# Kernel optimization log

Measured on AMD Instinct MI355X. Metric: run time of the kernel, lower is better.

Reference implementation:

```python
import jax, jax.numpy as jnp
import numpy as np

B, S, D = 2, 4096, 512   # batch, seq_len, input_dim
W, H = 256, 4            # memory width (d_model), attention heads
DH = W // H              # per-head depth


def _dense(x, w, b):
    return x @ w + b


def setup_inputs() -> dict:
    key = jax.random.key(0)
    ks = jax.random.split(key, 24)
    def w(k, shape):
        return jax.random.normal(k, shape, dtype=jnp.float32) * 0.02
    inp = {
        "x": jax.random.normal(ks[0], (B, S, D), dtype=jnp.float32),
        # outer q/k/v projections D -> W
        "qp_w": w(ks[1], (D, W)), "qp_b": jnp.zeros((W,), jnp.float32),
        "kp_w": w(ks[2], (D, W)), "kp_b": jnp.zeros((W,), jnp.float32),
        "vp_w": w(ks[3], (D, W)), "vp_b": jnp.zeros((W,), jnp.float32),
        # MHA internal projections W -> W
        "wq_w": w(ks[4], (W, W)), "wq_b": jnp.zeros((W,), jnp.float32),
        "wk_w": w(ks[5], (W, W)), "wk_b": jnp.zeros((W,), jnp.float32),
        "wv_w": w(ks[6], (W, W)), "wv_b": jnp.zeros((W,), jnp.float32),
        "wo_w": w(ks[7], (W, W)), "wo_b": jnp.zeros((W,), jnp.float32),
        # deep MLP memory (depth=2, gelu) + its output proj W -> W
        "m0_w": w(ks[8], (W, W)), "m0_b": jnp.zeros((W,), jnp.float32),
        "m1_w": w(ks[9], (W, W)), "m1_b": jnp.zeros((W,), jnp.float32),
        "mo_w": w(ks[10], (W, W)), "mo_b": jnp.zeros((W,), jnp.float32),
        # final output projection W -> D
        "op_w": w(ks[11], (W, D)), "op_b": jnp.zeros((D,), jnp.float32),
    }
    return inp


def reference(x, qp_w, qp_b, kp_w, kp_b, vp_w, vp_b,
              wq_w, wq_b, wk_w, wk_b, wv_w, wv_b, wo_w, wo_b,
              m0_w, m0_b, m1_w, m1_b, mo_w, mo_b, op_w, op_b):
    # outer projections (D -> W)
    q0 = _dense(x, qp_w, qp_b)
    k0 = _dense(x, kp_w, kp_b)
    v0 = _dense(x, vp_w, vp_b)
    # MHA internal projections (W -> W)
    q = _dense(q0, wq_w, wq_b)
    k = _dense(k0, wk_w, wk_b)
    v = _dense(v0, wv_w, wv_b)
    # split heads: [B,S,W] -> [B,H,S,DH]
    def split(t):
        return t.reshape(B, S, H, DH).transpose(0, 2, 1, 3)
    qh, kh, vh = split(q), split(k), split(v)
    scores = jnp.einsum('bhqd,bhkd->bhqk', qh, kh) / jnp.sqrt(jnp.float32(DH))
    attn = jax.nn.softmax(scores, axis=-1)
    ctx = jnp.einsum('bhqk,bhkd->bhqd', attn, vh)
    ctx = ctx.transpose(0, 2, 1, 3).reshape(B, S, W)
    retrieved = _dense(ctx, wo_w, wo_b)
    # deep MLP memory (exact gelu, matching keras 'gelu')
    h = jax.nn.gelu(_dense(retrieved, m0_w, m0_b), approximate=False)
    h = jax.nn.gelu(_dense(h, m1_w, m1_b), approximate=False)
    mem = _dense(h, mo_w, mo_b)
    # final projection + residual
    out = _dense(mem, op_w, op_b) + x
    return out
```

## Files before the change

kernel.cpp:

```cpp
#include <hip/hip_runtime.h>
#include <cstdint>
#include <cstddef>


#define GAS(p) ((const __attribute__((address_space(1))) void*)(p))
#define LAS(p) ((__attribute__((address_space(3))) void*)(p))

typedef __attribute__((ext_vector_type(8))) short bfrag;
typedef __attribute__((ext_vector_type(4))) float facc;
typedef __attribute__((ext_vector_type(16))) float facc16;
typedef uint16_t u16;

__device__ __forceinline__ u16 f2bf(float f) {
  uint32_t u = __float_as_uint(f);
  u += 0x7fffu + ((u >> 16) & 1u);
  return (u16)(u >> 16);
}
__device__ __forceinline__ float bf2f(u16 h) {
  return __uint_as_float((uint32_t)h << 16);
}
__device__ __forceinline__ float fast_exp2(float x) {
  float r;
  asm("v_exp_f32 %0, %1" : "=v"(r) : "v"(x));
  return r;
}
__device__ __forceinline__ float fast_rcp(float x) {
  float r;
  asm("v_rcp_f32 %0, %1" : "=v"(r) : "v"(x));
  return r;
}
__device__ __forceinline__ float gelu_fast(float v) {
  float y = v * 0.7978845608028654f * (1.f + 0.044715f * v * v);
  float e = fast_exp2(y * 2.8853900817779268f);
  float t = (e - 1.f) * fast_rcp(e + 1.f);
  return 0.5f * v * (1.f + t);
}
__device__ __forceinline__ facc mfma16(bfrag a, bfrag b, facc c) {
  return __builtin_amdgcn_mfma_f32_16x16x32_bf16(a, b, c, 0, 0, 0);
}
__device__ __forceinline__ facc16 mfma32(bfrag a, bfrag b, facc16 c) {
  return __builtin_amdgcn_mfma_f32_32x32x16_bf16(a, b, c, 0, 0, 0);
}

union U4 { uint32_t w[4]; bfrag f; };

__device__ __forceinline__ bfrag lds_frag(const u16* lds, int row, int kk, int ln) {
  int kb  = (kk << 6) + ((ln >> 4) << 4);
  int off = (row << 7) + (kb ^ ((row & 7) << 4));
  return *(const bfrag*)((const char*)lds + off);
}

template <int ROWS, int NW>
__device__ __forceinline__ void stage_tile(const u16* gbase, int ldK, u16* lds,
                                           int wv, int ln) {
#pragma unroll
  for (int i = 0; i < ROWS / 8 / NW; i++) {
    int seg = i * NW + wv;
    int row = (seg << 3) + (ln >> 3);
    int kb  = (ln & 7) << 4;
    const char* g = (const char*)(gbase + (size_t)row * ldK) +
                    (kb ^ ((row & 7) << 4));
    __builtin_amdgcn_global_load_lds(GAS(g), LAS(lds + (seg << 9)), 16, 0, 0);
  }
}

template <int EPI, int BN>
__global__ __launch_bounds__(256) void gemm_bt(
    const u16* __restrict__ A, const u16* __restrict__ Bt,
    const float* __restrict__ bias, const float* __restrict__ resid,
    u16* __restrict__ obf, float* __restrict__ of32,
    u16* __restrict__ qb, u16* __restrict__ kb2, u16* __restrict__ vb,
    int M, int N, int K) {
  const int t = threadIdx.x, wv = t >> 6, ln = t & 63;
  const int wr = wv >> 1, wc = wv & 1;
  const int m0 = blockIdx.y << 7, n0 = blockIdx.x * BN;
  constexpr int NJ = (BN + 31) / 32;

  __shared__ __align__(16) u16 Al[128 * 64];
  __shared__ __align__(16) u16 Bl[BN * 64];

  facc acc[4][NJ];
#pragma unroll
  for (int i = 0; i < 4; i++)
#pragma unroll
    for (int j = 0; j < NJ; j++)
#pragma unroll
      for (int r = 0; r < 4; r++) acc[i][j][r] = 0.f;

  const u16* Ab = A + (size_t)m0 * K;
  const u16* Bb = Bt + (size_t)n0 * K;
  stage_tile<128, 4>(Ab, K, Al, wv, ln);
  stage_tile<BN, 4>(Bb, K, Bl, wv, ln);

  const int nk = K >> 6;
  for (int kt = 0; kt < nk; ++kt) {
    __syncthreads();
#pragma unroll
    for (int kk = 0; kk < 2; kk++) {
      bfrag av[4], bv[NJ];
#pragma unroll
      for (int i = 0; i < 4; i++)
        av[i] = lds_frag(Al, (wr << 6) + (i << 4) + (ln & 15), kk, ln);
#pragma unroll
      for (int j = 0; j < NJ; j++)
        bv[j] = lds_frag(Bl, wc * (BN / 2) + (j << 4) + (ln & 15), kk, ln);
      __builtin_amdgcn_s_setprio(1);
#pragma unroll
      for (int i = 0; i < 4; i++)
#pragma unroll
        for (int j = 0; j < NJ; j++)
          acc[i][j] = mfma16(av[i], bv[j], acc[i][j]);
      __builtin_amdgcn_s_setprio(0);
    }
    if (kt + 1 < nk) {
      __syncthreads();
      stage_tile<128, 4>(Ab + (kt + 1) * 64, K, Al, wv, ln);
      stage_tile<BN, 4>(Bb + (kt + 1) * 64, K, Bl, wv, ln);
    }
  }

  const int rb = (ln >> 4) << 2, cb = ln & 15;
#pragma unroll
  for (int i = 0; i < 4; i++) {
#pragma unroll
    for (int j = 0; j < NJ; j++) {
      const int col = n0 + wc * (BN / 2) + (j << 4) + cb;
      const float bcol = bias ? bias[col] : 0.f;
#pragma unroll
      for (int r = 0; r < 4; r++) {
        const int row = m0 + (wr << 6) + (i << 4) + rb + r;
        float val = acc[i][j][r] + bcol;
        if (EPI == 0) {
          obf[(size_t)row * N + col] = f2bf(val);
        } else if (EPI == 1) {
          obf[(size_t)row * N + col] = f2bf(gelu_fast(val));
        } else if (EPI == 2) {
          const int sec = col >> 8, cc = col & 255, h = cc >> 6, dh = cc & 63;
          const int b = row >> 12, s = row & 4095;
          const int bh = b * 4 + h;
          if (sec == 0) {
            qb[((size_t)bh * 4096 + s) * 64 + dh] =
                f2bf(val * 0.18033688011112042f);
          } else if (sec == 1) {
            const int kt2 = s >> 5, kl = s & 31;
            const int dc = dh >> 4, lane = kl + ((dh >> 3) & 1) * 32, e = dh & 7;
            kb2[((size_t)bh * 128 + kt2) * 2048 + dc * 512 + lane * 8 + e] =
                f2bf(val);
          } else {
            const int kt2 = s >> 5, c = (s >> 4) & 1;
            const int lane = ((s >> 3) & 1) * 32 + (dh & 31), e = s & 7;
            const int dj = dh >> 5;
            vb[((size_t)bh * 128 + kt2) * 2048 + (c * 2 + dj) * 512 +
               lane * 8 + e] = f2bf(val);
          }
        } else {
          of32[(size_t)row * N + col] = val + resid[(size_t)row * N + col];
        }
      }
    }
  }
}

__global__ __launch_bounds__(256) void wgemm5(
    const u16* __restrict__ wqkvT, const u16* __restrict__ owqkv,
    const u16* __restrict__ m0_t, const u16* __restrict__ wo_bf,
    const u16* __restrict__ opT, const u16* __restrict__ mo_bf,
    u16* __restrict__ Wqkv_t, u16* __restrict__ Wf1_t,
    u16* __restrict__ Wmo_t) {
  const int z = blockIdx.z;
  const u16 *A, *Bt; u16* out; int M, N, rowOff;
  if (z < 3)      { A = wqkvT + z * 65536; Bt = owqkv + z * 131072;
                    out = Wqkv_t; M = 256; N = 512; rowOff = z * 256; }
  else if (z == 3){ A = m0_t; Bt = wo_bf; out = Wf1_t; M = 256; N = 256; rowOff = 0; }
  else            { A = opT;  Bt = mo_bf; out = Wmo_t; M = 512; N = 256; rowOff = 0; }
  const int m0 = blockIdx.y << 7, n0 = blockIdx.x << 6;
  if (m0 >= M || n0 >= N) return;

  const int t = threadIdx.x, wv = t >> 6, ln = t & 63;
  const int wr = wv >> 1, wc = wv & 1;
  __shared__ __align__(16) u16 Al[128 * 64];
  __shared__ __align__(16) u16 Bl[64 * 64];

  facc acc[4][2];
#pragma unroll
  for (int i = 0; i < 4; i++)
#pragma unroll
    for (int j = 0; j < 2; j++)
#pragma unroll
      for (int r = 0; r < 4; r++) acc[i][j][r] = 0.f;

  const u16* Ab = A + (size_t)m0 * 256;
  const u16* Bb = Bt + (size_t)n0 * 256;
  stage_tile<128, 4>(Ab, 256, Al, wv, ln);
  stage_tile<64, 4>(Bb, 256, Bl, wv, ln);

  for (int kt = 0; kt < 4; ++kt) {
    __syncthreads();
#pragma unroll
    for (int kk = 0; kk < 2; kk++) {
      bfrag av[4], bv[2];
#pragma unroll
      for (int i = 0; i < 4; i++)
        av[i] = lds_frag(Al, (wr << 6) + (i << 4) + (ln & 15), kk, ln);
#pragma unroll
      for (int j = 0; j < 2; j++)
        bv[j] = lds_frag(Bl, wc * 32 + (j << 4) + (ln & 15), kk, ln);
#pragma unroll
      for (int i = 0; i < 4; i++)
#pragma unroll
        for (int j = 0; j < 2; j++)
          acc[i][j] = mfma16(av[i], bv[j], acc[i][j]);
    }
    if (kt + 1 < 4) {
      __syncthreads();
      stage_tile<128, 4>(Ab + (kt + 1) * 64, 256, Al, wv, ln);
      stage_tile<64, 4>(Bb + (kt + 1) * 64, 256, Bl, wv, ln);
    }
  }

  const int rb = (ln >> 4) << 2, cb = ln & 15;
#pragma unroll
  for (int i = 0; i < 4; i++)
#pragma unroll
    for (int j = 0; j < 2; j++) {
      const int col = n0 + wc * 32 + (j << 4) + cb;
#pragma unroll
      for (int r = 0; r < 4; r++) {
        const int row = m0 + (wr << 6) + (i << 4) + rb + r;
        out[(size_t)(rowOff + row) * N + col] = f2bf(acc[i][j][r]);
      }
    }
}

__global__ __launch_bounds__(128) void attn5(
    const u16* __restrict__ qg, const u16* __restrict__ kfg,
    const u16* __restrict__ vfg, u16* __restrict__ Opart,
    float* __restrict__ lpart, int NT) {
  const int t = threadIdx.x, wv = t >> 6, ln = t & 63;
  const int l31 = ln & 31, lh = ln >> 5;
  const int qt = blockIdx.x, bh = blockIdx.y, kv = blockIdx.z;
  const int qbase = qt * 128 + wv * 64;
  const u16* Q  = qg + ((size_t)bh * 4096 + qbase) * 64;
  const u16* Kf = kfg + ((size_t)bh * 128 + (size_t)kv * NT) * 2048;
  const u16* Vf = vfg + ((size_t)bh * 128 + (size_t)kv * NT) * 2048;

  __shared__ __align__(16) u16 Klds[2][2048];
  __shared__ __align__(16) u16 Vlds[2][2048];

  bfrag qf[2][4];
#pragma unroll
  for (int qi = 0; qi < 2; qi++) {
    const u16* qp = Q + (size_t)(((qi << 5) + l31) << 6) + (lh << 3);
#pragma unroll
    for (int dc = 0; dc < 4; dc++)
      qf[qi][dc] = *(const bfrag*)(qp + (dc << 4));
  }

  facc16 oacc[2][2];
#pragma unroll
  for (int qi = 0; qi < 2; qi++)
#pragma unroll
    for (int r = 0; r < 16; r++) { oacc[qi][0][r] = 0.f; oacc[qi][1][r] = 0.f; }
  float lsum0 = 0.f, lsum1 = 0.f;

  {
    const u16* src = wv ? Vf : Kf;
    u16* dst = wv ? Vlds[0] : Klds[0];
#pragma unroll
    for (int i = 0; i < 4; i++)
      __builtin_amdgcn_global_load_lds(GAS(src + i * 512 + ln * 8),
                                       LAS(dst + i * 512), 16, 0, 0);
  }

  for (int kt = 0; kt < NT; ++kt) {
    const int cur = kt & 1;
    __syncthreads();
    if (kt + 1 < NT) {
      const u16* src = (wv ? Vf : Kf) + (size_t)(kt + 1) * 2048;
      u16* dst = wv ? Vlds[cur ^ 1] : Klds[cur ^ 1];
#pragma unroll
      for (int i = 0; i < 4; i++)
        __builtin_amdgcn_global_load_lds(GAS(src + i * 512 + ln * 8),
                                         LAS(dst + i * 512), 16, 0, 0);
    }
    bfrag kf[4];
#pragma unroll
    for (int dc = 0; dc < 4; dc++)
      kf[dc] = *(const bfrag*)(Klds[cur] + dc * 512 + ln * 8);

    bfrag pa[2][2];
#pragma unroll
    for (int qi = 0; qi < 2; qi++) {
      facc16 sa;
#pragma unroll
      for (int r = 0; r < 16; r++) sa[r] = 0.f;
      __builtin_amdgcn_s_setprio(1);
#pragma unroll
      for (int dc = 0; dc < 4; dc++)
        sa = mfma32(kf[dc], qf[qi][dc], sa);
      __builtin_amdgcn_s_setprio(0);
      float p[16];
      float ls = 0.f;
#pragma unroll
      for (int r = 0; r < 16; r++) { p[r] = fast_exp2(sa[r]); ls += p[r]; }
      if (qi == 0) lsum0 += ls; else lsum1 += ls;
      uint32_t u0, u1, u2, u3, u4, u5, u6, u7;
      asm("v_cvt_pk_bf16_f32 %0, %1, %2" : "=v"(u0) : "v"(p[0]),  "v"(p[1]));
      asm("v_cvt_pk_bf16_f32 %0, %1, %2" : "=v"(u1) : "v"(p[2]),  "v"(p[3]));
      asm("v_cvt_pk_bf16_f32 %0, %1, %2" : "=v"(u2) : "v"(p[4]),  "v"(p[5]));
      asm("v_cvt_pk_bf16_f32 %0, %1, %2" : "=v"(u3) : "v"(p[6]),  "v"(p[7]));
      asm("v_cvt_pk_bf16_f32 %0, %1, %2" : "=v"(u4) : "v"(p[8]),  "v"(p[9]));
      asm("v_cvt_pk_bf16_f32 %0, %1, %2" : "=v"(u5) : "v"(p[10]), "v"(p[11]));
      asm("v_cvt_pk_bf16_f32 %0, %1, %2" : "=v"(u6) : "v"(p[12]), "v"(p[13]));
      asm("v_cvt_pk_bf16_f32 %0, %1, %2" : "=v"(u7) : "v"(p[14]), "v"(p[15]));
      asm volatile("v_permlane32_swap_b32 %0, %1" : "+v"(u0), "+v"(u2));
      asm volatile("v_permlane32_swap_b32 %0, %1" : "+v"(u1), "+v"(u3));
      asm volatile("v_permlane32_swap_b32 %0, %1" : "+v"(u4), "+v"(u6));
      asm volatile("v_permlane32_swap_b32 %0, %1" : "+v"(u5), "+v"(u7));
      U4 c0; c0.w[0] = u0; c0.w[1] = u1; c0.w[2] = u2; c0.w[3] = u3;
      U4 c1; c1.w[0] = u4; c1.w[1] = u5; c1.w[2] = u6; c1.w[3] = u7;
      pa[qi][0] = c0.f;
      pa[qi][1] = c1.f;
    }
#pragma unroll
    for (int c = 0; c < 2; c++) {
      bfrag vf0 = *(const bfrag*)(Vlds[cur] + (c * 2 + 0) * 512 + ln * 8);
      bfrag vf1 = *(const bfrag*)(Vlds[cur] + (c * 2 + 1) * 512 + ln * 8);
      __builtin_amdgcn_s_setprio(1);
      oacc[0][0] = mfma32(pa[0][c], vf0, oacc[0][0]);
      oacc[1][0] = mfma32(pa[1][c], vf0, oacc[1][0]);
      oacc[0][1] = mfma32(pa[0][c], vf1, oacc[0][1]);
      oacc[1][1] = mfma32(pa[1][c], vf1, oacc[1][1]);
      __builtin_amdgcn_s_setprio(0);
    }
  }

  lsum0 += __shfl_xor(lsum0, 32);
  lsum1 += __shfl_xor(lsum1, 32);

  const size_t obase = ((size_t)kv * 8 + bh) * 4096 + qbase;
#pragma unroll
  for (int qi = 0; qi < 2; qi++) {
#pragma unroll
    for (int r = 0; r < 16; r++) {
      const int qrow = (qi << 5) + (r & 3) + ((r >> 2) << 3) + (lh << 2);
#pragma unroll
      for (int dj = 0; dj < 2; dj++)
        Opart[(obase + qrow) * 64 + (dj << 5) + l31] = f2bf(oacc[qi][dj][r]);
    }
    if (lh == 0)
      lpart[obase + (qi << 5) + l31] = qi == 0 ? lsum0 : lsum1;
  }
}

__global__ __launch_bounds__(256) void attn_combineN(
    const u16* __restrict__ Opart, const float* __restrict__ lpart,
    u16* __restrict__ ctx, int np) {
  const int idx = blockIdx.x * 256 + threadIdx.x;
  const int d0 = (idx & 7) << 3, s = (idx >> 3) & 4095, bh = idx >> 15;
  const size_t sb = (size_t)bh * 4096 + s;
  float acc[8] = {0.f, 0.f, 0.f, 0.f, 0.f, 0.f, 0.f, 0.f};
  float lsum = 0.f;
  for (int pz = 0; pz < np; pz++) {
    const size_t pb = (size_t)pz * 8 * 4096;
    bfrag a = *(const bfrag*)(Opart + (pb + sb) * 64 + d0);
#pragma unroll
    for (int j = 0; j < 8; j++) acc[j] += bf2f((u16)a[j]);
    lsum += lpart[pb + sb];
  }
  const float rl = 1.f / lsum;
  bfrag o;
#pragma unroll
  for (int j = 0; j < 8; j++) o[j] = (short)f2bf(acc[j] * rl);
  *(bfrag*)(ctx + ((size_t)(bh >> 2) * 4096 + s) * 256 + ((bh & 3) << 6) + d0) = o;
}

__global__ __launch_bounds__(256) void prep_all(
    const float* __restrict__ x,
    const float* __restrict__ qp, const float* __restrict__ kp,
    const float* __restrict__ vp, const float* __restrict__ mo,
    const float* __restrict__ wo,
    const float* __restrict__ wq, const float* __restrict__ wk,
    const float* __restrict__ wv, const float* __restrict__ m0,
    const float* __restrict__ m1, const float* __restrict__ op_w,
    const float* __restrict__ qp_b, const float* __restrict__ kp_b,
    const float* __restrict__ vp_b, const float* __restrict__ wq_b,
    const float* __restrict__ wk_b, const float* __restrict__ wv_b,
    const float* __restrict__ mo_b, const float* __restrict__ op_b,
    const float* __restrict__ wo_b, const float* __restrict__ m0_b,
    u16* __restrict__ xb, u16* __restrict__ owqkv, u16* __restrict__ mo_bf,
    u16* __restrict__ wo_bf, u16* __restrict__ wqkvT, u16* __restrict__ m0_t,
    u16* __restrict__ m1_t, u16* __restrict__ opT,
    float* __restrict__ bqkv, float* __restrict__ bmo,
    float* __restrict__ bf1) {
  const int bid = blockIdx.x, t = threadIdx.x;
  if (bid < 2048) {
    const size_t i = ((size_t)bid * 256 + t) * 8;
    float4 a = *(const float4*)(x + i);
    float4 b = *(const float4*)(x + i + 4);
    bfrag o;
    o[0] = (short)f2bf(a.x); o[1] = (short)f2bf(a.y);
    o[2] = (short)f2bf(a.z); o[3] = (short)f2bf(a.w);
    o[4] = (short)f2bf(b.x); o[5] = (short)f2bf(b.y);
    o[6] = (short)f2bf(b.z); o[7] = (short)f2bf(b.w);
    *(bfrag*)(xb + i) = o;
  } else if (bid < 2176) {
    const int i = (bid - 2048) * 4096 + t * 16;
    const float* s; u16* dst; int off;
    if (i < 131072)      { s = qp; dst = owqkv;          off = i; }
    else if (i < 262144) { s = kp; dst = owqkv + 131072; off = i - 131072; }
    else if (i < 393216) { s = vp; dst = owqkv + 262144; off = i - 262144; }
    else if (i < 458752) { s = mo; dst = mo_bf;          off = i - 393216; }
    else                 { s = wo; dst = wo_bf;          off = i - 458752; }
    bfrag o0, o1;
#pragma unroll
    for (int q = 0; q < 2; q++) {
      float4 v0 = *(const float4*)(s + off + q * 8);
      float4 v1 = *(const float4*)(s + off + q * 8 + 4);
      bfrag& o = q ? o1 : o0;
      o[0] = (short)f2bf(v0.x); o[1] = (short)f2bf(v0.y);
      o[2] = (short)f2bf(v0.z); o[3] = (short)f2bf(v0.w);
      o[4] = (short)f2bf(v1.x); o[5] = (short)f2bf(v1.y);
      o[6] = (short)f2bf(v1.z); o[7] = (short)f2bf(v1.w);
    }
    *(bfrag*)(dst + off) = o0;
    *(bfrag*)(dst + off + 8) = o1;
  } else if (bid < 2288) {
    __shared__ float tile[64][65];
    const int tid = bid - 2176;
    const float* src; u16* dst; int r0, c0, ldS, ldD;
    if (tid < 80) {
      const int mi = tid >> 4, tt = tid & 15;
      r0 = ((tt >> 2) << 6); c0 = ((tt & 3) << 6); ldS = 256; ldD = 256;
      switch (mi) {
        case 0: src = wq; dst = wqkvT; break;
        case 1: src = wk; dst = wqkvT + 65536; break;
        case 2: src = wv; dst = wqkvT + 131072; break;
        case 3: src = m0; dst = m0_t; break;
        default: src = m1; dst = m1_t; break;
      }
    } else {
      const int tt = tid - 80;
      r0 = ((tt >> 3) << 6); c0 = ((tt & 7) << 6);
      ldS = 512; ldD = 256; src = op_w; dst = opT;
    }
    {
      const int r = t >> 2, cc = (t & 3) << 4;
      const float* sp = src + (size_t)(r0 + r) * ldS + c0 + cc;
#pragma unroll
      for (int q = 0; q < 4; q++) {
        float4 v = *(const float4*)(sp + q * 4);
        tile[r][cc + q * 4 + 0] = v.x; tile[r][cc + q * 4 + 1] = v.y;
        tile[r][cc + q * 4 + 2] = v.z; tile[r][cc + q * 4 + 3] = v.w;
      }
    }
    __syncthreads();
    {
      const int cl = t >> 2, k16 = (t & 3) << 4;
      bfrag o0, o1;
#pragma unroll
      for (int j = 0; j < 8; j++) {
        o0[j] = (short)f2bf(tile[k16 + j][cl]);
        o1[j] = (short)f2bf(tile[k16 + 8 + j][cl]);
      }
      u16* dp = dst + (size_t)(c0 + cl) * ldD + r0 + k16;
      *(bfrag*)(dp) = o0;
      *(bfrag*)(dp + 8) = o1;
    }
  } else {
    const int bz = bid - 2288;
    if (bz < 3) {
      const float* ob = bz == 0 ? qp_b : (bz == 1 ? kp_b : vp_b);
      const float* iw = bz == 0 ? wq : (bz == 1 ? wk : wv);
      const float* ib = bz == 0 ? wq_b : (bz == 1 ? wk_b : wv_b);
      float s = 0.f;
      for (int c = 0; c < 256; c++) s += ob[c] * iw[(size_t)c * 256 + t];
      bqkv[bz * 256 + t] = s + ib[t];
    } else if (bz < 5) {
      const int d = (bz - 3) * 256 + t;
      float s = 0.f;
      for (int c = 0; c < 256; c++) s += mo_b[c] * op_w[(size_t)c * 512 + d];
      bmo[d] = s + op_b[d];
    } else {
      float s = 0.f;
      for (int c = 0; c < 256; c++) s += wo_b[c] * m0[(size_t)c * 256 + t];
      bf1[t] = s + m0_b[t];
    }
  }
}

extern "C" void kernel_launch(void* const* d_in, const int* in_sizes, int n_in,
                              void* d_out, int out_size, void* d_ws,
                              size_t ws_size, hipStream_t stream) {
  const float* x    = (const float*)d_in[0];
  const float* qp_w = (const float*)d_in[1];
  const float* qp_b = (const float*)d_in[2];
  const float* kp_w = (const float*)d_in[3];
  const float* kp_b = (const float*)d_in[4];
  const float* vp_w = (const float*)d_in[5];
  const float* vp_b = (const float*)d_in[6];
  const float* wq_w = (const float*)d_in[7];
  const float* wq_b = (const float*)d_in[8];
  const float* wk_w = (const float*)d_in[9];
  const float* wk_b = (const float*)d_in[10];
  const float* wv_w = (const float*)d_in[11];
  const float* wv_b = (const float*)d_in[12];
  const float* wo_w = (const float*)d_in[13];
  const float* wo_b = (const float*)d_in[14];
  const float* m0_w = (const float*)d_in[15];
  const float* m0_b = (const float*)d_in[16];
  const float* m1_w = (const float*)d_in[17];
  const float* m1_b = (const float*)d_in[18];
  const float* mo_w = (const float*)d_in[19];
  const float* mo_b = (const float*)d_in[20];
  const float* op_w = (const float*)d_in[21];
  const float* op_b = (const float*)d_in[22];
  float* out = (float*)d_out;

  const size_t MB = 1024 * 1024;
  const int kvs = (ws_size >= 56 * MB) ? 8 : 4;
  const int NT = 128 / kvs;

  char* ws = (char*)d_ws;
  u16*   q_buf  = (u16*)(ws);
  u16*   kf_buf = (u16*)(ws + 4 * MB);
  u16*   vf_buf = (u16*)(ws + 8 * MB);
  u16*   ctx    = (u16*)(ws + 12 * MB);
  u16*   xb     = (u16*)(ws + 16 * MB);
  u16*   Opart  = (u16*)(ws + 16 * MB);
  char*  wb     = ws + 16 * MB + (size_t)kvs * 4 * MB;
  u16*   owqkv  = (u16*)(wb);
  u16*   wqkvT  = (u16*)(wb + 786432);
  u16*   Wqkv_t = (u16*)(wb + 1179648);
  u16*   m0_t   = (u16*)(wb + 1966080);
  u16*   m1_t   = (u16*)(wb + 2097152);
  u16*   opT    = (u16*)(wb + 2228224);
  u16*   mo_bf  = (u16*)(wb + 2490368);
  u16*   wo_bf  = (u16*)(wb + 2621440);
  u16*   Wf1_t  = (u16*)(wb + 2752512);
  u16*   Wmo_t  = (u16*)(wb + 2883584);
  float* bqkv   = (float*)(wb + 3145728);
  float* bmo    = (float*)(wb + 3149824);
  float* bf1    = (float*)(wb + 3151872);
  float* lpart  = (float*)(wb + 3153920);
  u16* h1 = q_buf;
  u16* h2 = kf_buf;

  prep_all<<<2294, 256, 0, stream>>>(
      x, qp_w, kp_w, vp_w, mo_w, wo_w,
      wq_w, wk_w, wv_w, m0_w, m1_w, op_w,
      qp_b, kp_b, vp_b, wq_b, wk_b, wv_b, mo_b, op_b, wo_b, m0_b,
      xb, owqkv, mo_bf, wo_bf, wqkvT, m0_t, m1_t, opT, bqkv, bmo, bf1);
  wgemm5<<<dim3(8, 4, 5), 256, 0, stream>>>(
      wqkvT, owqkv, m0_t, wo_bf, opT, mo_bf, Wqkv_t, Wf1_t, Wmo_t);

  gemm_bt<2, 64><<<dim3(12, 64), 256, 0, stream>>>(
      xb, Wqkv_t, bqkv, nullptr, nullptr, nullptr, q_buf, kf_buf, vf_buf,
      8192, 768, 512);
  attn5<<<dim3(32, 8, kvs), 128, 0, stream>>>(q_buf, kf_buf, vf_buf,
                                              Opart, lpart, NT);
  attn_combineN<<<1024, 256, 0, stream>>>(Opart, lpart, ctx, kvs);

  gemm_bt<1, 32><<<dim3(8, 64), 256, 0, stream>>>(
      ctx, Wf1_t, bf1, nullptr, h1, nullptr, nullptr, nullptr, nullptr,
      8192, 256, 256);
  gemm_bt<1, 32><<<dim3(8, 64), 256, 0, stream>>>(
      h1, m1_t, m1_b, nullptr, h2, nullptr, nullptr, nullptr, nullptr,
      8192, 256, 256);
  gemm_bt<3, 64><<<dim3(8, 64), 256, 0, stream>>>(
      h2, Wmo_t, bmo, x, nullptr, out, nullptr, nullptr, nullptr,
      8192, 512, 256);
}
```

Before: 223.1 us.

## Use single-wave attention blocks with vmcnt waits and MFMA row sums

Each attention block is reduced from two waves to one. That single wave now loads both its K and V tiles into LDS itself, and __syncthreads is replaced by explicit s_waitcnt vmcnt counting for the double buffer. The softmax row sums are no longer accumulated with VALU adds and a cross-lane shuffle; they come from extra MFMAs of P against a ones fragment, which also changes how lpart is written. This removes block barriers and VALU work but doubles the grid, and each block now issues more loads per wave and duplicates the K/V LDS traffic.

```diff
diff --git a/kernel.cpp b/kernel.cpp
--- a/kernel.cpp
+++ b/kernel.cpp
@@ -232,14 +232,14 @@
     }
 }
 
-__global__ __launch_bounds__(128) void attn5(
+__global__ __launch_bounds__(64) void attn7(
     const u16* __restrict__ qg, const u16* __restrict__ kfg,
     const u16* __restrict__ vfg, u16* __restrict__ Opart,
     float* __restrict__ lpart, int NT) {
-  const int t = threadIdx.x, wv = t >> 6, ln = t & 63;
+  const int ln = threadIdx.x;
   const int l31 = ln & 31, lh = ln >> 5;
   const int qt = blockIdx.x, bh = blockIdx.y, kv = blockIdx.z;
-  const int qbase = qt * 128 + wv * 64;
+  const int qbase = qt * 64;
   const u16* Q  = qg + ((size_t)bh * 4096 + qbase) * 64;
   const u16* Kf = kfg + ((size_t)bh * 128 + (size_t)kv * NT) * 2048;
   const u16* Vf = vfg + ((size_t)bh * 128 + (size_t)kv * NT) * 2048;
@@ -255,34 +255,47 @@
     for (int dc = 0; dc < 4; dc++)
       qf[qi][dc] = *(const bfrag*)(qp + (dc << 4));
   }
+  bfrag ones;
+#pragma unroll
+  for (int j = 0; j < 8; j++) ones[j] = (short)0x3F80;
 
   facc16 oacc[2][2];
+  facc16 lacc[2];
 #pragma unroll
   for (int qi = 0; qi < 2; qi++)
 #pragma unroll
-    for (int r = 0; r < 16; r++) { oacc[qi][0][r] = 0.f; oacc[qi][1][r] = 0.f; }
-  float lsum0 = 0.f, lsum1 = 0.f;
-
-  {
-    const u16* src = wv ? Vf : Kf;
-    u16* dst = wv ? Vlds[0] : Klds[0];
-#pragma unroll
-    for (int i = 0; i < 4; i++)
-      __builtin_amdgcn_global_load_lds(GAS(src + i * 512 + ln * 8),
-                                       LAS(dst + i * 512), 16, 0, 0);
-  }
+    for (int r = 0; r < 16; r++) {
+      oacc[qi][0][r] = 0.f; oacc[qi][1][r] = 0.f; lacc[qi][r] = 0.f;
+    }
+
+#pragma unroll
+  for (int i = 0; i < 4; i++)
+    __builtin_amdgcn_global_load_lds(GAS(Kf + i * 512 + ln * 8),
+                                     LAS(Klds[0] + i * 512), 16, 0, 0);
+#pragma unroll
+  for (int i = 0; i < 4; i++)
+    __builtin_amdgcn_global_load_lds(GAS(Vf + i * 512 + ln * 8),
+                                     LAS(Vlds[0] + i * 512), 16, 0, 0);
 
   for (int kt = 0; kt < NT; ++kt) {
     const int cur = kt & 1;
-    __syncthreads();
     if (kt + 1 < NT) {
-      const u16* src = (wv ? Vf : Kf) + (size_t)(kt + 1) * 2048;
-      u16* dst = wv ? Vlds[cur ^ 1] : Klds[cur ^ 1];
+      const u16* ksrc = Kf + (size_t)(kt + 1) * 2048;
+      const u16* vsrc = Vf + (size_t)(kt + 1) * 2048;
 #pragma unroll
       for (int i = 0; i < 4; i++)
-        __builtin_amdgcn_global_load_lds(GAS(src + i * 512 + ln * 8),
-                                         LAS(dst + i * 512), 16, 0, 0);
-    }
+        __builtin_amdgcn_global_load_lds(GAS(ksrc + i * 512 + ln * 8),
+                                         LAS(Klds[cur ^ 1] + i * 512), 16, 0, 0);
+#pragma unroll
+      for (int i = 0; i < 4; i++)
+        __builtin_amdgcn_global_load_lds(GAS(vsrc + i * 512 + ln * 8),
+                                         LAS(Vlds[cur ^ 1] + i * 512), 16, 0, 0);
+      asm volatile("s_waitcnt vmcnt(8)" ::: "memory");
+    } else {
+      asm volatile("s_waitcnt vmcnt(0)" ::: "memory");
+    }
+    __builtin_amdgcn_sched_barrier(0);
+
     bfrag kf[4];
 #pragma unroll
     for (int dc = 0; dc < 4; dc++)
@@ -300,10 +313,8 @@
         sa = mfma32(kf[dc], qf[qi][dc], sa);
       __builtin_amdgcn_s_setprio(0);
       float p[16];
-      float ls = 0.f;
-#pragma unroll
-      for (int r = 0; r < 16; r++) { p[r] = fast_exp2(sa[r]); ls += p[r]; }
-      if (qi == 0) lsum0 += ls; else lsum1 += ls;
+#pragma unroll
+      for (int r = 0; r < 16; r++) p[r] = fast_exp2(sa[r]);
       uint32_t u0, u1, u2, u3, u4, u5, u6, u7;
       asm("v_cvt_pk_bf16_f32 %0, %1, %2" : "=v"(u0) : "v"(p[0]),  "v"(p[1]));
       asm("v_cvt_pk_bf16_f32 %0, %1, %2" : "=v"(u1) : "v"(p[2]),  "v"(p[3]));
@@ -331,12 +342,11 @@
       oacc[1][0] = mfma32(pa[1][c], vf0, oacc[1][0]);
       oacc[0][1] = mfma32(pa[0][c], vf1, oacc[0][1]);
       oacc[1][1] = mfma32(pa[1][c], vf1, oacc[1][1]);
+      lacc[0] = mfma32(pa[0][c], ones, lacc[0]);
+      lacc[1] = mfma32(pa[1][c], ones, lacc[1]);
       __builtin_amdgcn_s_setprio(0);
     }
   }
-
-  lsum0 += __shfl_xor(lsum0, 32);
-  lsum1 += __shfl_xor(lsum1, 32);
 
   const size_t obase = ((size_t)kv * 8 + bh) * 4096 + qbase;
 #pragma unroll
@@ -347,9 +357,8 @@
 #pragma unroll
       for (int dj = 0; dj < 2; dj++)
         Opart[(obase + qrow) * 64 + (dj << 5) + l31] = f2bf(oacc[qi][dj][r]);
-    }
-    if (lh == 0)
-      lpart[obase + (qi << 5) + l31] = qi == 0 ? lsum0 : lsum1;
+      if (l31 == 0) lpart[obase + qrow] = lacc[qi][r];
+    }
   }
 }
 
@@ -557,8 +566,8 @@
   gemm_bt<2, 64><<<dim3(12, 64), 256, 0, stream>>>(
       xb, Wqkv_t, bqkv, nullptr, nullptr, nullptr, q_buf, kf_buf, vf_buf,
       8192, 768, 512);
-  attn5<<<dim3(32, 8, kvs), 128, 0, stream>>>(q_buf, kf_buf, vf_buf,
-                                              Opart, lpart, NT);
+  attn7<<<dim3(64, 8, kvs), 64, 0, stream>>>(q_buf, kf_buf, vf_buf,
+                                             Opart, lpart, NT);
   attn_combineN<<<1024, 256, 0, stream>>>(Opart, lpart, ctx, kvs);
 
   gemm_bt<1, 32><<<dim3(8, 64), 256, 0, stream>>>(
```

Result: slower. 229.5 us (+2.9%).

## Replace LDS-staged attention with single-wave kernel loading K/V fragments directly to registers

Applied to the files above, without the earlier changes.

The attention kernel drops its shared-memory double buffer and block barriers. Each single-wavefront block now loads K and V fragments straight from global memory into registers, with a two-deep register ping-pong that prefetches the next tile while the current one is computed. The grid doubles in the query dimension so each block still covers 64 queries. This removes the LDS round trip and __syncthreads, but K/V are no longer shared between two waves, so global/L2 traffic for K/V doubles and register pressure rises. The loop also assumes NT is even, since the second step in each iteration runs unconditionally.

```diff
diff --git a/kernel.cpp b/kernel.cpp
--- a/kernel.cpp
+++ b/kernel.cpp
@@ -232,21 +232,75 @@
     }
 }
 
-__global__ __launch_bounds__(128) void attn5(
+#define LOAD_KV(kf_, vf_, kt_)                                               \
+  do {                                                                       \
+    const u16* kp_ = Kf + (size_t)(kt_) * 2048 + (ln << 3);                  \
+    const u16* vp_ = Vf + (size_t)(kt_) * 2048 + (ln << 3);                  \
+    _Pragma("unroll")                                                        \
+    for (int i_ = 0; i_ < 4; i_++) kf_[i_] = *(const bfrag*)(kp_ + i_ * 512);\
+    _Pragma("unroll")                                                        \
+    for (int i_ = 0; i_ < 4; i_++) vf_[i_] = *(const bfrag*)(vp_ + i_ * 512);\
+  } while (0)
+
+#define ATTN_TILE_STEP(kf_, vf_)                                             \
+  do {                                                                       \
+    bfrag pa[2][2];                                                          \
+    _Pragma("unroll")                                                        \
+    for (int qi = 0; qi < 2; qi++) {                                         \
+      facc16 sa;                                                             \
+      _Pragma("unroll")                                                      \
+      for (int r = 0; r < 16; r++) sa[r] = 0.f;                              \
+      __builtin_amdgcn_s_setprio(1);                                         \
+      _Pragma("unroll")                                                      \
+      for (int dc = 0; dc < 4; dc++)                                         \
+        sa = mfma32(kf_[dc], qf[qi][dc], sa);                                \
+      __builtin_amdgcn_s_setprio(0);                                         \
+      float p[16];                                                           \
+      float ls = 0.f;                                                        \
+      _Pragma("unroll")                                                      \
+      for (int r = 0; r < 16; r++) { p[r] = fast_exp2(sa[r]); ls += p[r]; }  \
+      if (qi == 0) lsum0 += ls; else lsum1 += ls;                            \
+      uint32_t u0, u1, u2, u3, u4, u5, u6, u7;                               \
+      asm("v_cvt_pk_bf16_f32 %0, %1, %2" : "=v"(u0) : "v"(p[0]),  "v"(p[1]));\
+      asm("v_cvt_pk_bf16_f32 %0, %1, %2" : "=v"(u1) : "v"(p[2]),  "v"(p[3]));\
+      asm("v_cvt_pk_bf16_f32 %0, %1, %2" : "=v"(u2) : "v"(p[4]),  "v"(p[5]));\
+      asm("v_cvt_pk_bf16_f32 %0, %1, %2" : "=v"(u3) : "v"(p[6]),  "v"(p[7]));\
+      asm("v_cvt_pk_bf16_f32 %0, %1, %2" : "=v"(u4) : "v"(p[8]),  "v"(p[9]));\
+      asm("v_cvt_pk_bf16_f32 %0, %1, %2" : "=v"(u5) : "v"(p[10]), "v"(p[11]));\
+      asm("v_cvt_pk_bf16_f32 %0, %1, %2" : "=v"(u6) : "v"(p[12]), "v"(p[13]));\
+      asm("v_cvt_pk_bf16_f32 %0, %1, %2" : "=v"(u7) : "v"(p[14]), "v"(p[15]));\
+      asm volatile("v_permlane32_swap_b32 %0, %1" : "+v"(u0), "+v"(u2));     \
+      asm volatile("v_permlane32_swap_b32 %0, %1" : "+v"(u1), "+v"(u3));     \
+      asm volatile("v_permlane32_swap_b32 %0, %1" : "+v"(u4), "+v"(u6));     \
+      asm volatile("v_permlane32_swap_b32 %0, %1" : "+v"(u5), "+v"(u7));     \
+      U4 c0; c0.w[0] = u0; c0.w[1] = u1; c0.w[2] = u2; c0.w[3] = u3;         \
+      U4 c1; c1.w[0] = u4; c1.w[1] = u5; c1.w[2] = u6; c1.w[3] = u7;         \
+      pa[qi][0] = c0.f;                                                      \
+      pa[qi][1] = c1.f;                                                      \
+    }                                                                        \
+    _Pragma("unroll")                                                        \
+    for (int c = 0; c < 2; c++) {                                            \
+      __builtin_amdgcn_s_setprio(1);                                         \
+      oacc[0][0] = mfma32(pa[0][c], vf_[c * 2 + 0], oacc[0][0]);             \
+      oacc[1][0] = mfma32(pa[1][c], vf_[c * 2 + 0], oacc[1][0]);             \
+      oacc[0][1] = mfma32(pa[0][c], vf_[c * 2 + 1], oacc[0][1]);             \
+      oacc[1][1] = mfma32(pa[1][c], vf_[c * 2 + 1], oacc[1][1]);             \
+      __builtin_amdgcn_s_setprio(0);                                         \
+    }                                                                        \
+  } while (0)
+
+__global__ __launch_bounds__(64) void attn8(
     const u16* __restrict__ qg, const u16* __restrict__ kfg,
     const u16* __restrict__ vfg, u16* __restrict__ Opart,
     float* __restrict__ lpart, int NT) {
-  const int t = threadIdx.x, wv = t >> 6, ln = t & 63;
+  const int ln = threadIdx.x;
   const int l31 = ln & 31, lh = ln >> 5;
   const int qt = blockIdx.x, bh = blockIdx.y, kv = blockIdx.z;
-  const int qbase = qt * 128 + wv * 64;
+  const int qbase = qt * 64;
   const u16* Q  = qg + ((size_t)bh * 4096 + qbase) * 64;
   const u16* Kf = kfg + ((size_t)bh * 128 + (size_t)kv * NT) * 2048;
   const u16* Vf = vfg + ((size_t)bh * 128 + (size_t)kv * NT) * 2048;
 
-  __shared__ __align__(16) u16 Klds[2][2048];
-  __shared__ __align__(16) u16 Vlds[2][2048];
-
   bfrag qf[2][4];
 #pragma unroll
   for (int qi = 0; qi < 2; qi++) {
@@ -263,76 +317,13 @@
     for (int r = 0; r < 16; r++) { oacc[qi][0][r] = 0.f; oacc[qi][1][r] = 0.f; }
   float lsum0 = 0.f, lsum1 = 0.f;
 
-  {
-    const u16* src = wv ? Vf : Kf;
-    u16* dst = wv ? Vlds[0] : Klds[0];
-#pragma unroll
-    for (int i = 0; i < 4; i++)
-      __builtin_amdgcn_global_load_lds(GAS(src + i * 512 + ln * 8),
-                                       LAS(dst + i * 512), 16, 0, 0);
-  }
-
-  for (int kt = 0; kt < NT; ++kt) {
-    const int cur = kt & 1;
-    __syncthreads();
-    if (kt + 1 < NT) {
-      const u16* src = (wv ? Vf : Kf) + (size_t)(kt + 1) * 2048;
-      u16* dst = wv ? Vlds[cur ^ 1] : Klds[cur ^ 1];
-#pragma unroll
-      for (int i = 0; i < 4; i++)
-        __builtin_amdgcn_global_load_lds(GAS(src + i * 512 + ln * 8),
-                                         LAS(dst + i * 512), 16, 0, 0);
-    }
-    bfrag kf[4];
-#pragma unroll
-    for (int dc = 0; dc < 4; dc++)
-      kf[dc] = *(const bfrag*)(Klds[cur] + dc * 512 + ln * 8);
-
-    bfrag pa[2][2];
-#pragma unroll
-    for (int qi = 0; qi < 2; qi++) {
-      facc16 sa;
-#pragma unroll
-      for (int r = 0; r < 16; r++) sa[r] = 0.f;
-      __builtin_amdgcn_s_setprio(1);
-#pragma unroll
-      for (int dc = 0; dc < 4; dc++)
-        sa = mfma32(kf[dc], qf[qi][dc], sa);
-      __builtin_amdgcn_s_setprio(0);
-      float p[16];
-      float ls = 0.f;
-#pragma unroll
-      for (int r = 0; r < 16; r++) { p[r] = fast_exp2(sa[r]); ls += p[r]; }
-      if (qi == 0) lsum0 += ls; else lsum1 += ls;
-      uint32_t u0, u1, u2, u3, u4, u5, u6, u7;
-      asm("v_cvt_pk_bf16_f32 %0, %1, %2" : "=v"(u0) : "v"(p[0]),  "v"(p[1]));
-      asm("v_cvt_pk_bf16_f32 %0, %1, %2" : "=v"(u1) : "v"(p[2]),  "v"(p[3]));
-      asm("v_cvt_pk_bf16_f32 %0, %1, %2" : "=v"(u2) : "v"(p[4]),  "v"(p[5]));
-      asm("v_cvt_pk_bf16_f32 %0, %1, %2" : "=v"(u3) : "v"(p[6]),  "v"(p[7]));
-      asm("v_cvt_pk_bf16_f32 %0, %1, %2" : "=v"(u4) : "v"(p[8]),  "v"(p[9]));
-      asm("v_cvt_pk_bf16_f32 %0, %1, %2" : "=v"(u5) : "v"(p[10]), "v"(p[11]));
-      asm("v_cvt_pk_bf16_f32 %0, %1, %2" : "=v"(u6) : "v"(p[12]), "v"(p[13]));
-      asm("v_cvt_pk_bf16_f32 %0, %1, %2" : "=v"(u7) : "v"(p[14]), "v"(p[15]));
-      asm volatile("v_permlane32_swap_b32 %0, %1" : "+v"(u0), "+v"(u2));
-      asm volatile("v_permlane32_swap_b32 %0, %1" : "+v"(u1), "+v"(u3));
-      asm volatile("v_permlane32_swap_b32 %0, %1" : "+v"(u4), "+v"(u6));
-      asm volatile("v_permlane32_swap_b32 %0, %1" : "+v"(u5), "+v"(u7));
-      U4 c0; c0.w[0] = u0; c0.w[1] = u1; c0.w[2] = u2; c0.w[3] = u3;
-      U4 c1; c1.w[0] = u4; c1.w[1] = u5; c1.w[2] = u6; c1.w[3] = u7;
-      pa[qi][0] = c0.f;
-      pa[qi][1] = c1.f;
-    }
-#pragma unroll
-    for (int c = 0; c < 2; c++) {
-      bfrag vf0 = *(const bfrag*)(Vlds[cur] + (c * 2 + 0) * 512 + ln * 8);
-      bfrag vf1 = *(const bfrag*)(Vlds[cur] + (c * 2 + 1) * 512 + ln * 8);
-      __builtin_amdgcn_s_setprio(1);
-      oacc[0][0] = mfma32(pa[0][c], vf0, oacc[0][0]);
-      oacc[1][0] = mfma32(pa[1][c], vf0, oacc[1][0]);
-      oacc[0][1] = mfma32(pa[0][c], vf1, oacc[0][1]);
-      oacc[1][1] = mfma32(pa[1][c], vf1, oacc[1][1]);
-      __builtin_amdgcn_s_setprio(0);
-    }
+  bfrag ka[4], va[4], kb[4], vb[4];
+  LOAD_KV(ka, va, 0);
+  for (int kt = 0; kt < NT; kt += 2) {
+    LOAD_KV(kb, vb, kt + 1);
+    ATTN_TILE_STEP(ka, va);
+    if (kt + 2 < NT) LOAD_KV(ka, va, kt + 2);
+    ATTN_TILE_STEP(kb, vb);
   }
 
   lsum0 += __shfl_xor(lsum0, 32);
@@ -557,8 +548,8 @@
   gemm_bt<2, 64><<<dim3(12, 64), 256, 0, stream>>>(
       xb, Wqkv_t, bqkv, nullptr, nullptr, nullptr, q_buf, kf_buf, vf_buf,
       8192, 768, 512);
-  attn5<<<dim3(32, 8, kvs), 128, 0, stream>>>(q_buf, kf_buf, vf_buf,
-                                              Opart, lpart, NT);
+  attn8<<<dim3(64, 8, kvs), 64, 0, stream>>>(q_buf, kf_buf, vf_buf,
+                                             Opart, lpart, NT);
   attn_combineN<<<1024, 256, 0, stream>>>(Opart, lpart, ctx, kvs);
 
   gemm_bt<1, 32><<<dim3(8, 64), 256, 0, stream>>>(
```

New measurement: 219.2 us. About the same (-1.7%).
